# Optimization experiments

Hardware: AMD Instinct MI355X
Metric: run time of the kernel (lower is better)

The kernel has to match this reference:

```python
import jax, jax.numpy as jnp
import numpy as np

H = 128
B, N, K = 2, 16384, 16


def _gather_neighbors(a, idx):
    # a: (B,N,D), idx: (B,N,K) -> (B,N,K,D), per-batch gather along N
    return jax.vmap(lambda ab, ib: ab[ib])(a, idx)


def setup_inputs() -> dict:
    key = jax.random.key(0)
    ks = jax.random.split(key, 16)
    def lin(k, fan_in, shape):
        lim = 1.0 / np.sqrt(fan_in)
        return jax.random.uniform(k, shape, jnp.float32, -lim, lim)
    inp = {
        'h': jax.random.normal(ks[0], (B, N, H), jnp.float32),
        'x': jax.random.normal(ks[1], (B, N, 3), jnp.float32),
        'edge_idx': jax.random.randint(ks[2], (B, N, K), 0, N),
        # edge_mlp: Linear(2H+1->H), SiLU, Linear(H->H), SiLU
        'We1': lin(ks[3], 2 * H + 1, (2 * H + 1, H)), 'be1': lin(ks[4], 2 * H + 1, (H,)),
        'We2': lin(ks[5], H, (H, H)), 'be2': lin(ks[6], H, (H,)),
        # coord_mlp: Linear(H->H), SiLU, Linear(H->1, no bias)
        'Wc1': lin(ks[7], H, (H, H)), 'bc1': lin(ks[8], H, (H,)),
        'Wc2': lin(ks[9], H, (H, 1)),
        # node_mlp: Linear(2H->H), SiLU, Linear(H->H)
        'Wn1': lin(ks[10], 2 * H, (2 * H, H)), 'bn1': lin(ks[11], 2 * H, (H,)),
        'Wn2': lin(ks[12], H, (H, H)), 'bn2': lin(ks[13], H, (H,)),
    }
    return inp


def reference(h, x, edge_idx, We1, be1, We2, be2, Wc1, bc1, Wc2, Wn1, bn1, Wn2, bn2):
    k = edge_idx.shape[2]
    h_neigh = _gather_neighbors(h, edge_idx)          # (B,N,K,H)
    x_neigh = _gather_neighbors(x, edge_idx)          # (B,N,K,3)
    x_diff = x[:, :, None, :] - x_neigh               # (B,N,K,3)
    sq_dist = jnp.sum(x_diff * x_diff, axis=-1, keepdims=True)  # (B,N,K,1)
    h_i = jnp.broadcast_to(h[:, :, None, :], h_neigh.shape)
    edge_feat = jnp.concatenate([h_i, h_neigh, sq_dist], axis=-1)  # (B,N,K,2H+1)
    m_ij = jax.nn.silu(jax.nn.silu(edge_feat @ We1 + be1) @ We2 + be2)  # (B,N,K,H)
    coord_w = jax.nn.silu(m_ij @ Wc1 + bc1) @ Wc2     # (B,N,K,1)
    x_new = x + jnp.mean(x_diff * coord_w, axis=2)    # (B,N,3)
    m_i = jnp.sum(m_ij, axis=2)                       # (B,N,H)
    node_in = jnp.concatenate([h, m_i], axis=-1)      # (B,N,2H)
    h_new = jax.nn.silu(node_in @ Wn1 + bn1) @ Wn2 + bn2 + h
    return (h_new, x_new)
```

## Files before the change

### kernel.cpp

```cpp
#include <hip/hip_runtime.h>
#include <hip/hip_bf16.h>
#include <math.h>

#define H 128
#define KN 16
#define NN 16384
#define NB 8
#define EB 128
#define HS 136

typedef short s16x8 __attribute__((ext_vector_type(8)));
typedef float f32x4 __attribute__((ext_vector_type(4)));

__device__ __forceinline__ float u2f_lo(uint u){
    union { uint i; float f; } v; v.i = u << 16; return v.f;
}
__device__ __forceinline__ float u2f_hi(uint u){
    union { uint i; float f; } v; v.i = u & 0xffff0000u; return v.f;
}
__device__ __forceinline__ uint pk2(float lo, float hi){
    __hip_bfloat162 b = __float22bfloat162_rn(float2{lo, hi});
    uint u; __builtin_memcpy(&u, &b, 4); return u;
}
__device__ __forceinline__ ushort f2b1(float f){
    __hip_bfloat16 b = __float2bfloat16(f);
    ushort u; __builtin_memcpy(&u, &b, 2); return u;
}
__device__ __forceinline__ float silu_f(float v){
    float e = __expf(-v);
    return v * __builtin_amdgcn_rcpf(1.0f + e);
}

__global__ __launch_bounds__(256) void pack_all(
    const float* __restrict__ We2, const float* __restrict__ Wc1,
    const float* __restrict__ Wn1, const float* __restrict__ Wn2,
    const float* __restrict__ We1,
    ushort* __restrict__ dWe2, ushort* __restrict__ dWc1,
    ushort* __restrict__ dWn1, ushort* __restrict__ dWn2,
    ushort* __restrict__ dW1p)
{
    int idx = blockIdx.x * 256 + threadIdx.x;
    int fid = idx >> 6, l = idx & 63;
    const float* src; ushort* dst; int Kt; int mode = 0; int lfid;
    if (fid < 32)       { src = We2; dst = dWe2; Kt = 4; lfid = fid; }
    else if (fid < 64)  { src = Wc1; dst = dWc1; Kt = 4; lfid = fid - 32; }
    else if (fid < 128) { src = Wn1; dst = dWn1; Kt = 8; lfid = fid - 64; }
    else if (fid < 160) { src = Wn2; dst = dWn2; Kt = 4; lfid = fid - 128; }
    else                { src = We1; dst = dW1p; Kt = 4; mode = 1; lfid = fid - 160; }
    int mt = lfid / Kt, kt = lfid % Kt;
    int m = mt * 16 + (l & 15);
    s16x8 ov;
#pragma unroll
    for (int e = 0; e < 8; e++){
        int k = kt * 32 + ((l >> 4) << 3) + e;
        float v;
        if (mode == 0) v = src[k * 128 + m];
        else           v = src[(k + ((m >= 128) ? 128 : 0)) * 128 + (m & 127)];
        ov[e] = (short)f2b1(v);
    }
    *(s16x8*)(dst + (size_t)lfid * 512 + l * 8) = ov;
}

__global__ __launch_bounds__(256) void precompute_mfma(
    const float* __restrict__ h, const float* __restrict__ be1,
    const ushort* __restrict__ W1p,
    ushort* __restrict__ A, ushort* __restrict__ Bm)
{
    const int tid = threadIdx.x;
    const int w = tid >> 6, l = tid & 63, lg = l >> 4, li = l & 15;
    const int i0 = blockIdx.x * 64;

    f32x4 acc[4][4];
#pragma unroll
    for (int a = 0; a < 4; a++)
#pragma unroll
        for (int b = 0; b < 4; b++){ acc[a][b][0]=0.f; acc[a][b][1]=0.f; acc[a][b][2]=0.f; acc[a][b][3]=0.f; }

    for (int nt = 0; nt < 4; nt++){
        int node = i0 + nt * 16 + li;
        const float* hp = h + (size_t)node * 128 + lg * 8;
        s16x8 bfr[4];
#pragma unroll
        for (int kt = 0; kt < 4; kt++){
            float4 v0 = *(const float4*)(hp + kt * 32);
            float4 v1 = *(const float4*)(hp + kt * 32 + 4);
            uint4 uu = make_uint4(pk2(v0.x, v0.y), pk2(v0.z, v0.w),
                                  pk2(v1.x, v1.y), pk2(v1.z, v1.w));
            s16x8 bf; __builtin_memcpy(&bf, &uu, 16);
            bfr[kt] = bf;
        }
#pragma unroll
        for (int mtl = 0; mtl < 4; mtl++){
            int mt = w * 4 + mtl;
#pragma unroll
            for (int kt = 0; kt < 4; kt++){
                s16x8 af = *(const s16x8*)(W1p + (size_t)(mt * 4 + kt) * 512 + l * 8);
                acc[mtl][nt] = __builtin_amdgcn_mfma_f32_16x16x32_bf16(af, bfr[kt], acc[mtl][nt], 0, 0, 0);
            }
        }
    }
#pragma unroll
    for (int mtl = 0; mtl < 4; mtl++){
        int mt = w * 4 + mtl;
        int ccb = mt * 16 + lg * 4;
#pragma unroll
        for (int nt = 0; nt < 4; nt++){
            int node = i0 + nt * 16 + li;
            float b0=0.f,b1=0.f,b2=0.f,b3=0.f;
            if (ccb < 128){ float4 bb = *(const float4*)(be1 + ccb); b0=bb.x; b1=bb.y; b2=bb.z; b3=bb.w; }
            uint2 val = make_uint2(pk2(acc[mtl][nt][0] + b0, acc[mtl][nt][1] + b1),
                                   pk2(acc[mtl][nt][2] + b2, acc[mtl][nt][3] + b3));
            ushort* dst = (ccb < 128) ? (A + (size_t)node * 128 + ccb)
                                      : (Bm + (size_t)node * 128 + (ccb - 128));
            *(uint2*)dst = val;
        }
    }
}

__global__ __launch_bounds__(256, 4) void egnn_fused(
    const float* __restrict__ h, const float* __restrict__ x,
    const int* __restrict__ edge_idx,
    const ushort* __restrict__ A, const ushort* __restrict__ Bm,
    const float* __restrict__ We1,
    const ushort* __restrict__ We2T, const float* __restrict__ be2,
    const ushort* __restrict__ Wc1T, const float* __restrict__ bc1,
    const float* __restrict__ Wc2,
    const ushort* __restrict__ Wn1T, const float* __restrict__ bn1,
    const ushort* __restrict__ Wn2T, const float* __restrict__ bn2,
    float* __restrict__ out, int BN)
{
    __shared__ __align__(16) ushort m_lds[EB * 128];
    __shared__ __align__(16) uint   AshCw[512];
    __shared__ __align__(16) ushort hsh_bf[NB * HS];
    __shared__ __align__(16) ushort msum_bf[NB * HS];
    __shared__ __align__(16) ushort w256sh[128];
    __shared__ float  sqd[EB];
    __shared__ int    jgs[EB];

    ushort* Ash = (ushort*)AshCw;
    float (*cwvp)[EB] = (float(*)[EB])AshCw;

    const int tid = threadIdx.x;
    const int w = tid >> 6, l = tid & 63, lg = l >> 4, li = l & 15;
    const int i0 = blockIdx.x * NB;

    {
        int r = tid >> 5, c = (tid & 31) * 4;
        float4 hv = *(const float4*)&h[(size_t)(i0 + r) * 128 + c];
        *(uint2*)&hsh_bf[r * HS + c] = make_uint2(pk2(hv.x, hv.y), pk2(hv.z, hv.w));
        if (tid < 128){
            int rr = tid >> 4, cc = (tid & 15) * 8;
            *(uint4*)&Ash[rr * 128 + cc] = *(const uint4*)&A[(size_t)(i0 + rr) * 128 + cc];
        } else {
            int t2 = tid - 128;
            w256sh[t2] = f2b1(We1[256 * 128 + t2]);
        }
        if (tid < EB){
            int e = tid;
            int i = i0 + (e >> 4);
            int b = i / NN;
            int jl = edge_idx[(size_t)i * KN + (e & 15)];
            int j = b * NN + jl;
            jgs[e] = j;
            float d0 = x[(size_t)i*3+0] - x[(size_t)j*3+0];
            float d1 = x[(size_t)i*3+1] - x[(size_t)j*3+1];
            float d2 = x[(size_t)i*3+2] - x[(size_t)j*3+2];
            sqd[e] = d0*d0 + d1*d1 + d2*d2;
        }
    }
    __syncthreads();

    {
        const int e0 = w * 32;
#pragma unroll
        for (int nt = 0; nt < 2; nt++){
            int edge = e0 + nt * 16 + li;
            int nodel = edge >> 4;
            int j = jgs[edge];
            float sq = sqd[edge];
#pragma unroll
            for (int kt = 0; kt < 4; kt++){
                int c8 = kt * 32 + lg * 8;
                uint4 ub = *(const uint4*)&Bm[(size_t)j * 128 + c8];
                uint4 ua = *(const uint4*)&Ash[nodel * 128 + c8];
                uint4 uw = *(const uint4*)&w256sh[c8];
                uint ov[4];
                const uint* pa = (const uint*)&ua;
                const uint* pb = (const uint*)&ub;
                const uint* pw = (const uint*)&uw;
#pragma unroll
                for (int p = 0; p < 4; p++){
                    float tlo = fmaf(sq, u2f_lo(pw[p]), u2f_lo(pa[p]) + u2f_lo(pb[p]));
                    float thi = fmaf(sq, u2f_hi(pw[p]), u2f_hi(pa[p]) + u2f_hi(pb[p]));
                    ov[p] = pk2(silu_f(tlo), silu_f(thi));
                }
                int blk = (kt * 4 + lg) ^ (edge & 7);
                *(uint4*)&m_lds[edge * 128 + blk * 8] = make_uint4(ov[0], ov[1], ov[2], ov[3]);
            }
        }
    }
    __syncthreads();

    f32x4 acc[16];
#pragma unroll
    for (int q = 0; q < 16; q++){ acc[q][0]=0.f; acc[q][1]=0.f; acc[q][2]=0.f; acc[q][3]=0.f; }

    __builtin_amdgcn_s_setprio(1);
#pragma unroll
    for (int kt = 0; kt < 4; kt++){
        s16x8 bfr[8];
#pragma unroll
        for (int nt = 0; nt < 8; nt++){
            int edge = nt * 16 + li;
            int blk = (kt * 4 + lg) ^ (edge & 7);
            bfr[nt] = *(const s16x8*)&m_lds[edge * 128 + blk * 8];
        }
#pragma unroll
        for (int mtl = 0; mtl < 2; mtl++){
            int mt = w * 2 + mtl;
            s16x8 af = *(const s16x8*)&We2T[(size_t)(mt * 4 + kt) * 512 + l * 8];
#pragma unroll
            for (int nt = 0; nt < 8; nt++)
                acc[mtl * 8 + nt] = __builtin_amdgcn_mfma_f32_16x16x32_bf16(af, bfr[nt], acc[mtl * 8 + nt], 0, 0, 0);
        }
    }
    __builtin_amdgcn_s_setprio(0);
    __syncthreads();

#pragma unroll
    for (int mtl = 0; mtl < 2; mtl++){
        int mt = w * 2 + mtl;
        int cb = mt * 16 + lg * 4;
        float4 bb = *(const float4*)&be2[cb];
#pragma unroll
        for (int nt = 0; nt < 8; nt++){
            int edge = nt * 16 + li;
            f32x4 a = acc[mtl * 8 + nt];
            uint2 val = make_uint2(pk2(silu_f(a[0] + bb.x), silu_f(a[1] + bb.y)),
                                   pk2(silu_f(a[2] + bb.z), silu_f(a[3] + bb.w)));
            int blk = (mt * 2 + (lg >> 1)) ^ (edge & 7);
            *(uint2*)&m_lds[edge * 128 + blk * 8 + (lg & 1) * 4] = val;
        }
    }
    __syncthreads();
    {
        int nodel = l >> 3;
        int c0 = w * 32 + (l & 7) * 4;
        float s0=0.f, s1=0.f, s2=0.f, s3=0.f;
#pragma unroll
        for (int k = 0; k < 16; k++){
            int edge = nodel * 16 + k;
            int blk = (c0 >> 3) ^ (edge & 7);
            uint2 v = *(uint2*)&m_lds[edge * 128 + blk * 8 + (c0 & 4)];
            s0 += u2f_lo(v.x); s1 += u2f_hi(v.x);
            s2 += u2f_lo(v.y); s3 += u2f_hi(v.y);
        }
        *(uint2*)&msum_bf[nodel * HS + c0] = make_uint2(pk2(s0, s1), pk2(s2, s3));
    }
    __syncthreads();

#pragma unroll
    for (int q = 0; q < 16; q++){ acc[q][0]=0.f; acc[q][1]=0.f; acc[q][2]=0.f; acc[q][3]=0.f; }
    __builtin_amdgcn_s_setprio(1);
#pragma unroll
    for (int kt = 0; kt < 4; kt++){
        s16x8 bfr[8];
#pragma unroll
        for (int nt = 0; nt < 8; nt++){
            int edge = nt * 16 + li;
            int blk = (kt * 4 + lg) ^ (edge & 7);
            bfr[nt] = *(const s16x8*)&m_lds[edge * 128 + blk * 8];
        }
#pragma unroll
        for (int mtl = 0; mtl < 2; mtl++){
            int mt = w * 2 + mtl;
            s16x8 af = *(const s16x8*)&Wc1T[(size_t)(mt * 4 + kt) * 512 + l * 8];
#pragma unroll
            for (int nt = 0; nt < 8; nt++)
                acc[mtl * 8 + nt] = __builtin_amdgcn_mfma_f32_16x16x32_bf16(af, bfr[nt], acc[mtl * 8 + nt], 0, 0, 0);
        }
    }
    __builtin_amdgcn_s_setprio(0);
    __syncthreads();

    {
        float cwp[8];
#pragma unroll
        for (int nt = 0; nt < 8; nt++) cwp[nt] = 0.f;
#pragma unroll
        for (int mtl = 0; mtl < 2; mtl++){
            int mt = w * 2 + mtl;
            int cb = mt * 16 + lg * 4;
            float4 bc = *(const float4*)&bc1[cb];
            float4 wc = *(const float4*)&Wc2[cb];
#pragma unroll
            for (int nt = 0; nt < 8; nt++){
                f32x4 a = acc[mtl * 8 + nt];
                cwp[nt] += silu_f(a[0] + bc.x) * wc.x + silu_f(a[1] + bc.y) * wc.y
                         + silu_f(a[2] + bc.z) * wc.z + silu_f(a[3] + bc.w) * wc.w;
            }
        }
#pragma unroll
        for (int nt = 0; nt < 8; nt++){
            float v = cwp[nt];
            v += __shfl_xor(v, 16);
            v += __shfl_xor(v, 32);
            if (lg == 0) cwvp[w][nt * 16 + li] = v;
        }
    }

    {
        f32x4 acc3[2];
        acc3[0][0]=0.f; acc3[0][1]=0.f; acc3[0][2]=0.f; acc3[0][3]=0.f;
        acc3[1][0]=0.f; acc3[1][1]=0.f; acc3[1][2]=0.f; acc3[1][3]=0.f;
        int node = li & 7;
#pragma unroll
        for (int kt = 0; kt < 8; kt++){
            const ushort* bp = (kt < 4) ? &hsh_bf[node * HS + kt * 32 + lg * 8]
                                        : &msum_bf[node * HS + (kt - 4) * 32 + lg * 8];
            s16x8 bf = *(const s16x8*)bp;
#pragma unroll
            for (int mtl = 0; mtl < 2; mtl++){
                int mt = w * 2 + mtl;
                s16x8 af = *(const s16x8*)&Wn1T[(size_t)(mt * 8 + kt) * 512 + l * 8];
                acc3[mtl] = __builtin_amdgcn_mfma_f32_16x16x32_bf16(af, bf, acc3[mtl], 0, 0, 0);
            }
        }
#pragma unroll
        for (int mtl = 0; mtl < 2; mtl++){
            int mt = w * 2 + mtl;
            int cb = mt * 16 + lg * 4;
            float4 bb = *(const float4*)&bn1[cb];
            uint o01 = 0, o23 = 0;
            if (li < 8){
                f32x4 a = acc3[mtl];
                o01 = pk2(silu_f(a[0] + bb.x), silu_f(a[1] + bb.y));
                o23 = pk2(silu_f(a[2] + bb.z), silu_f(a[3] + bb.w));
            }
            int blk = (mt * 2 + (lg >> 1)) ^ (li & 7);
            *(uint2*)&m_lds[li * 128 + blk * 8 + (lg & 1) * 4] = make_uint2(o01, o23);
        }
    }
    __syncthreads();

    if (tid < 24){
        int nd = tid / 3, d = tid % 3;
        int i = i0 + nd;
        float xi = x[(size_t)i * 3 + d];
        float s = 0.f;
#pragma unroll
        for (int k = 0; k < 16; k++){
            int e = nd * 16 + k;
            float cw = cwvp[0][e] + cwvp[1][e] + cwvp[2][e] + cwvp[3][e];
            s += (xi - x[(size_t)jgs[e] * 3 + d]) * cw;
        }
        out[(size_t)BN * H + (size_t)i * 3 + d] = xi + s * (1.0f / 16.0f);
    }

    {
        f32x4 acc4[2];
        acc4[0][0]=0.f; acc4[0][1]=0.f; acc4[0][2]=0.f; acc4[0][3]=0.f;
        acc4[1][0]=0.f; acc4[1][1]=0.f; acc4[1][2]=0.f; acc4[1][3]=0.f;
#pragma unroll
        for (int kt = 0; kt < 4; kt++){
            int blk = (kt * 4 + lg) ^ (li & 7);
            s16x8 bf = *(const s16x8*)&m_lds[li * 128 + blk * 8];
#pragma unroll
            for (int mtl = 0; mtl < 2; mtl++){
                int mt = w * 2 + mtl;
                s16x8 af = *(const s16x8*)&Wn2T[(size_t)(mt * 4 + kt) * 512 + l * 8];
                acc4[mtl] = __builtin_amdgcn_mfma_f32_16x16x32_bf16(af, bf, acc4[mtl], 0, 0, 0);
            }
        }
#pragma unroll
        for (int mtl = 0; mtl < 2; mtl++){
            int mt = w * 2 + mtl;
            int cb = mt * 16 + lg * 4;
            if (li < 8){
                float4 bb = *(const float4*)&bn2[cb];
                float4 hv = *(const float4*)&h[(size_t)(i0 + li) * 128 + cb];
                f32x4 a = acc4[mtl];
                float4 o;
                o.x = a[0] + bb.x + hv.x;
                o.y = a[1] + bb.y + hv.y;
                o.z = a[2] + bb.z + hv.z;
                o.w = a[3] + bb.w + hv.w;
                *(float4*)&out[(size_t)(i0 + li) * 128 + cb] = o;
            }
        }
    }
}

extern "C" void kernel_launch(void* const* d_in, const int* in_sizes, int n_in,
                              void* d_out, int out_size, void* d_ws, size_t ws_size,
                              hipStream_t stream) {
    const float* h        = (const float*)d_in[0];
    const float* x        = (const float*)d_in[1];
    const int*   edge_idx = (const int*)d_in[2];
    const float* We1      = (const float*)d_in[3];
    const float* be1      = (const float*)d_in[4];
    const float* We2      = (const float*)d_in[5];
    const float* be2      = (const float*)d_in[6];
    const float* Wc1      = (const float*)d_in[7];
    const float* bc1      = (const float*)d_in[8];
    const float* Wc2      = (const float*)d_in[9];
    const float* Wn1      = (const float*)d_in[10];
    const float* bn1      = (const float*)d_in[11];
    const float* Wn2      = (const float*)d_in[12];
    const float* bn2      = (const float*)d_in[13];
    float* out = (float*)d_out;

    const int BN = in_sizes[0] / H;

    ushort* A    = (ushort*)d_ws;
    ushort* Bm   = A + (size_t)BN * H;
    ushort* We2T = Bm + (size_t)BN * H;
    ushort* Wc1T = We2T + 32 * 512;
    ushort* Wn1T = Wc1T + 32 * 512;
    ushort* Wn2T = Wn1T + 64 * 512;
    ushort* W1pT = Wn2T + 32 * 512;

    pack_all<<<56, 256, 0, stream>>>(We2, Wc1, Wn1, Wn2, We1,
                                     We2T, Wc1T, Wn1T, Wn2T, W1pT);
    precompute_mfma<<<BN / 64, 256, 0, stream>>>(h, be1, W1pT, A, Bm);
    egnn_fused<<<BN / NB, 256, 0, stream>>>(h, x, edge_idx, A, Bm, We1,
                                            We2T, be2, Wc1T, bc1, Wc2,
                                            Wn1T, bn1, Wn2T, bn2, out, BN);
}
```

Measured before the change: 140.4 us.

## Make each wave own its edges end to end, removing block barriers

Each wave now handles 32 edges (two nodes) across the whole edge pipeline. It computes the first-layer activations straight into MFMA register fragments instead of staging them in LDS, runs all 8 output tiles for its own edges, and keeps its private slice of the message buffer. This removes most __syncthreads and the Ash/w256sh/jgs staging, at the cost of more accumulator registers per wave and reloading all weight tiles per wave. Coordinate differences are cached in LDS as bf16, and the residual h is read from the bf16 shared copy. Both lower the precision of the x and h outputs.

```diff
diff --git a/kernel.cpp b/kernel.cpp
--- a/kernel.cpp
+++ b/kernel.cpp
@@ -17,6 +17,9 @@
 }
 __device__ __forceinline__ float u2f_hi(uint u){
     union { uint i; float f; } v; v.i = u & 0xffff0000u; return v.f;
+}
+__device__ __forceinline__ float b2f(ushort u){
+    union { uint i; float f; } v; v.i = ((uint)u) << 16; return v.f;
 }
 __device__ __forceinline__ uint pk2(float lo, float hi){
     __hip_bfloat162 b = __float22bfloat162_rn(float2{lo, hi});
@@ -130,15 +133,10 @@
     float* __restrict__ out, int BN)
 {
     __shared__ __align__(16) ushort m_lds[EB * 128];
-    __shared__ __align__(16) uint   AshCw[512];
     __shared__ __align__(16) ushort hsh_bf[NB * HS];
     __shared__ __align__(16) ushort msum_bf[NB * HS];
-    __shared__ __align__(16) ushort w256sh[128];
-    __shared__ float  sqd[EB];
-    __shared__ int    jgs[EB];
-
-    ushort* Ash = (ushort*)AshCw;
-    float (*cwvp)[EB] = (float(*)[EB])AshCw;
+    __shared__ float  cwv[EB];
+    __shared__ ushort xdb[EB * 3];
 
     const int tid = threadIdx.x;
     const int w = tid >> 6, l = tid & 63, lg = l >> 4, li = l & 15;
@@ -148,166 +146,144 @@
         int r = tid >> 5, c = (tid & 31) * 4;
         float4 hv = *(const float4*)&h[(size_t)(i0 + r) * 128 + c];
         *(uint2*)&hsh_bf[r * HS + c] = make_uint2(pk2(hv.x, hv.y), pk2(hv.z, hv.w));
-        if (tid < 128){
-            int rr = tid >> 4, cc = (tid & 15) * 8;
-            *(uint4*)&Ash[rr * 128 + cc] = *(const uint4*)&A[(size_t)(i0 + rr) * 128 + cc];
-        } else {
-            int t2 = tid - 128;
-            w256sh[t2] = f2b1(We1[256 * 128 + t2]);
-        }
-        if (tid < EB){
-            int e = tid;
-            int i = i0 + (e >> 4);
-            int b = i / NN;
-            int jl = edge_idx[(size_t)i * KN + (e & 15)];
-            int j = b * NN + jl;
-            jgs[e] = j;
-            float d0 = x[(size_t)i*3+0] - x[(size_t)j*3+0];
-            float d1 = x[(size_t)i*3+1] - x[(size_t)j*3+1];
-            float d2 = x[(size_t)i*3+2] - x[(size_t)j*3+2];
-            sqd[e] = d0*d0 + d1*d1 + d2*d2;
-        }
-    }
-    __syncthreads();
-
-    {
-        const int e0 = w * 32;
-#pragma unroll
-        for (int nt = 0; nt < 2; nt++){
-            int edge = e0 + nt * 16 + li;
-            int nodel = edge >> 4;
-            int j = jgs[edge];
-            float sq = sqd[edge];
-#pragma unroll
-            for (int kt = 0; kt < 4; kt++){
-                int c8 = kt * 32 + lg * 8;
-                uint4 ub = *(const uint4*)&Bm[(size_t)j * 128 + c8];
-                uint4 ua = *(const uint4*)&Ash[nodel * 128 + c8];
-                uint4 uw = *(const uint4*)&w256sh[c8];
-                uint ov[4];
-                const uint* pa = (const uint*)&ua;
-                const uint* pb = (const uint*)&ub;
-                const uint* pw = (const uint*)&uw;
-#pragma unroll
-                for (int p = 0; p < 4; p++){
-                    float tlo = fmaf(sq, u2f_lo(pw[p]), u2f_lo(pa[p]) + u2f_lo(pb[p]));
-                    float thi = fmaf(sq, u2f_hi(pw[p]), u2f_hi(pa[p]) + u2f_hi(pb[p]));
-                    ov[p] = pk2(silu_f(tlo), silu_f(thi));
-                }
-                int blk = (kt * 4 + lg) ^ (edge & 7);
-                *(uint4*)&m_lds[edge * 128 + blk * 8] = make_uint4(ov[0], ov[1], ov[2], ov[3]);
-            }
-        }
-    }
-    __syncthreads();
-
-    f32x4 acc[16];
-#pragma unroll
-    for (int q = 0; q < 16; q++){ acc[q][0]=0.f; acc[q][1]=0.f; acc[q][2]=0.f; acc[q][3]=0.f; }
+    }
+    float sqv = 0.f; int jv = 0;
+    if (l < 32) {
+        int el = w * 32 + l;
+        int i = i0 + (el >> 4);
+        int b = i / NN;
+        int jl = edge_idx[(size_t)i * KN + (el & 15)];
+        int j = b * NN + jl;
+        jv = j;
+        float d0 = x[(size_t)i*3+0] - x[(size_t)j*3+0];
+        float d1 = x[(size_t)i*3+1] - x[(size_t)j*3+1];
+        float d2 = x[(size_t)i*3+2] - x[(size_t)j*3+2];
+        xdb[el*3+0] = f2b1(d0); xdb[el*3+1] = f2b1(d1); xdb[el*3+2] = f2b1(d2);
+        sqv = d0*d0 + d1*d1 + d2*d2;
+    }
+
+    s16x8 tfr[2][4];
+#pragma unroll
+    for (int nt = 0; nt < 2; nt++){
+        int els = nt * 16 + li;
+        float sq = __shfl(sqv, els);
+        int j = __shfl(jv, els);
+        const size_t arow = (size_t)(i0 + w * 2 + nt) * 128;
+#pragma unroll
+        for (int kt = 0; kt < 4; kt++){
+            int c8 = kt * 32 + lg * 8;
+            uint4 ua = *(const uint4*)&A[arow + c8];
+            uint4 ub = *(const uint4*)&Bm[(size_t)j * 128 + c8];
+            float4 w0 = *(const float4*)&We1[256*128 + c8];
+            float4 w1 = *(const float4*)&We1[256*128 + c8 + 4];
+            float wlo[4] = {w0.x, w0.z, w1.x, w1.z};
+            float whi[4] = {w0.y, w0.w, w1.y, w1.w};
+            const uint* pa = (const uint*)&ua;
+            const uint* pb = (const uint*)&ub;
+            uint ov[4];
+#pragma unroll
+            for (int p = 0; p < 4; p++){
+                float tlo = fmaf(sq, wlo[p], u2f_lo(pa[p]) + u2f_lo(pb[p]));
+                float thi = fmaf(sq, whi[p], u2f_hi(pa[p]) + u2f_hi(pb[p]));
+                ov[p] = pk2(silu_f(tlo), silu_f(thi));
+            }
+            __builtin_memcpy(&tfr[nt][kt], ov, 16);
+        }
+    }
+
+    f32x4 acc[8][2];
+#pragma unroll
+    for (int mt = 0; mt < 8; mt++)
+#pragma unroll
+        for (int nt = 0; nt < 2; nt++){ acc[mt][nt][0]=0.f; acc[mt][nt][1]=0.f; acc[mt][nt][2]=0.f; acc[mt][nt][3]=0.f; }
 
     __builtin_amdgcn_s_setprio(1);
 #pragma unroll
     for (int kt = 0; kt < 4; kt++){
-        s16x8 bfr[8];
-#pragma unroll
-        for (int nt = 0; nt < 8; nt++){
-            int edge = nt * 16 + li;
-            int blk = (kt * 4 + lg) ^ (edge & 7);
-            bfr[nt] = *(const s16x8*)&m_lds[edge * 128 + blk * 8];
-        }
-#pragma unroll
-        for (int mtl = 0; mtl < 2; mtl++){
-            int mt = w * 2 + mtl;
-            s16x8 af = *(const s16x8*)&We2T[(size_t)(mt * 4 + kt) * 512 + l * 8];
-#pragma unroll
-            for (int nt = 0; nt < 8; nt++)
-                acc[mtl * 8 + nt] = __builtin_amdgcn_mfma_f32_16x16x32_bf16(af, bfr[nt], acc[mtl * 8 + nt], 0, 0, 0);
+#pragma unroll
+        for (int mt = 0; mt < 8; mt++){
+            s16x8 af = *(const s16x8*)&We2T[(size_t)(mt*4+kt)*512 + l*8];
+            acc[mt][0] = __builtin_amdgcn_mfma_f32_16x16x32_bf16(af, tfr[0][kt], acc[mt][0], 0, 0, 0);
+            acc[mt][1] = __builtin_amdgcn_mfma_f32_16x16x32_bf16(af, tfr[1][kt], acc[mt][1], 0, 0, 0);
         }
     }
     __builtin_amdgcn_s_setprio(0);
-    __syncthreads();
-
-#pragma unroll
-    for (int mtl = 0; mtl < 2; mtl++){
-        int mt = w * 2 + mtl;
+
+    ushort* mreg = m_lds + w * 32 * 128;
+#pragma unroll
+    for (int mt = 0; mt < 8; mt++){
         int cb = mt * 16 + lg * 4;
         float4 bb = *(const float4*)&be2[cb];
 #pragma unroll
-        for (int nt = 0; nt < 8; nt++){
-            int edge = nt * 16 + li;
-            f32x4 a = acc[mtl * 8 + nt];
+        for (int nt = 0; nt < 2; nt++){
+            int el = nt * 16 + li;
+            f32x4 a = acc[mt][nt];
             uint2 val = make_uint2(pk2(silu_f(a[0] + bb.x), silu_f(a[1] + bb.y)),
                                    pk2(silu_f(a[2] + bb.z), silu_f(a[3] + bb.w)));
-            int blk = (mt * 2 + (lg >> 1)) ^ (edge & 7);
-            *(uint2*)&m_lds[edge * 128 + blk * 8 + (lg & 1) * 4] = val;
-        }
-    }
-    __syncthreads();
+            int blk = (mt * 2 + (lg >> 1)) ^ (el & 7);
+            *(uint2*)&mreg[el * 128 + blk * 8 + (lg & 1) * 4] = val;
+        }
+    }
+
     {
-        int nodel = l >> 3;
-        int c0 = w * 32 + (l & 7) * 4;
+        int nodel = l >> 5;
+        int c0 = (l & 31) * 4;
         float s0=0.f, s1=0.f, s2=0.f, s3=0.f;
 #pragma unroll
         for (int k = 0; k < 16; k++){
-            int edge = nodel * 16 + k;
-            int blk = (c0 >> 3) ^ (edge & 7);
-            uint2 v = *(uint2*)&m_lds[edge * 128 + blk * 8 + (c0 & 4)];
+            int row = nodel * 16 + k;
+            int blk = (c0 >> 3) ^ (row & 7);
+            uint2 v = *(const uint2*)&mreg[row * 128 + blk * 8 + (c0 & 4)];
             s0 += u2f_lo(v.x); s1 += u2f_hi(v.x);
             s2 += u2f_lo(v.y); s3 += u2f_hi(v.y);
         }
-        *(uint2*)&msum_bf[nodel * HS + c0] = make_uint2(pk2(s0, s1), pk2(s2, s3));
-    }
-    __syncthreads();
-
-#pragma unroll
-    for (int q = 0; q < 16; q++){ acc[q][0]=0.f; acc[q][1]=0.f; acc[q][2]=0.f; acc[q][3]=0.f; }
+        *(uint2*)&msum_bf[(w*2 + nodel) * HS + c0] = make_uint2(pk2(s0, s1), pk2(s2, s3));
+    }
+
+    f32x4 acc2[8][2];
+#pragma unroll
+    for (int mt = 0; mt < 8; mt++)
+#pragma unroll
+        for (int nt = 0; nt < 2; nt++){ acc2[mt][nt][0]=0.f; acc2[mt][nt][1]=0.f; acc2[mt][nt][2]=0.f; acc2[mt][nt][3]=0.f; }
+
     __builtin_amdgcn_s_setprio(1);
 #pragma unroll
     for (int kt = 0; kt < 4; kt++){
-        s16x8 bfr[8];
-#pragma unroll
-        for (int nt = 0; nt < 8; nt++){
-            int edge = nt * 16 + li;
-            int blk = (kt * 4 + lg) ^ (edge & 7);
-            bfr[nt] = *(const s16x8*)&m_lds[edge * 128 + blk * 8];
-        }
-#pragma unroll
-        for (int mtl = 0; mtl < 2; mtl++){
-            int mt = w * 2 + mtl;
-            s16x8 af = *(const s16x8*)&Wc1T[(size_t)(mt * 4 + kt) * 512 + l * 8];
-#pragma unroll
-            for (int nt = 0; nt < 8; nt++)
-                acc[mtl * 8 + nt] = __builtin_amdgcn_mfma_f32_16x16x32_bf16(af, bfr[nt], acc[mtl * 8 + nt], 0, 0, 0);
+        int blk0 = (kt*4 + lg) ^ (li & 7);
+        s16x8 bf0 = *(const s16x8*)&mreg[li * 128 + blk0 * 8];
+        int el1 = 16 + li;
+        int blk1 = (kt*4 + lg) ^ (el1 & 7);
+        s16x8 bf1 = *(const s16x8*)&mreg[el1 * 128 + blk1 * 8];
+#pragma unroll
+        for (int mt = 0; mt < 8; mt++){
+            s16x8 af = *(const s16x8*)&Wc1T[(size_t)(mt*4+kt)*512 + l*8];
+            acc2[mt][0] = __builtin_amdgcn_mfma_f32_16x16x32_bf16(af, bf0, acc2[mt][0], 0, 0, 0);
+            acc2[mt][1] = __builtin_amdgcn_mfma_f32_16x16x32_bf16(af, bf1, acc2[mt][1], 0, 0, 0);
         }
     }
     __builtin_amdgcn_s_setprio(0);
-    __syncthreads();
 
     {
-        float cwp[8];
-#pragma unroll
-        for (int nt = 0; nt < 8; nt++) cwp[nt] = 0.f;
-#pragma unroll
-        for (int mtl = 0; mtl < 2; mtl++){
-            int mt = w * 2 + mtl;
+        float cwp0 = 0.f, cwp1 = 0.f;
+#pragma unroll
+        for (int mt = 0; mt < 8; mt++){
             int cb = mt * 16 + lg * 4;
             float4 bc = *(const float4*)&bc1[cb];
             float4 wc = *(const float4*)&Wc2[cb];
-#pragma unroll
-            for (int nt = 0; nt < 8; nt++){
-                f32x4 a = acc[mtl * 8 + nt];
-                cwp[nt] += silu_f(a[0] + bc.x) * wc.x + silu_f(a[1] + bc.y) * wc.y
-                         + silu_f(a[2] + bc.z) * wc.z + silu_f(a[3] + bc.w) * wc.w;
-            }
-        }
-#pragma unroll
-        for (int nt = 0; nt < 8; nt++){
-            float v = cwp[nt];
-            v += __shfl_xor(v, 16);
-            v += __shfl_xor(v, 32);
-            if (lg == 0) cwvp[w][nt * 16 + li] = v;
-        }
-    }
+            f32x4 a0 = acc2[mt][0], a1 = acc2[mt][1];
+            cwp0 += silu_f(a0[0]+bc.x)*wc.x + silu_f(a0[1]+bc.y)*wc.y
+                  + silu_f(a0[2]+bc.z)*wc.z + silu_f(a0[3]+bc.w)*wc.w;
+            cwp1 += silu_f(a1[0]+bc.x)*wc.x + silu_f(a1[1]+bc.y)*wc.y
+                  + silu_f(a1[2]+bc.z)*wc.z + silu_f(a1[3]+bc.w)*wc.w;
+        }
+        cwp0 += __shfl_xor(cwp0, 16); cwp0 += __shfl_xor(cwp0, 32);
+        cwp1 += __shfl_xor(cwp1, 16); cwp1 += __shfl_xor(cwp1, 32);
+        if (lg == 0){
+            cwv[w*32 + li]      = cwp0;
+            cwv[w*32 + 16 + li] = cwp1;
+        }
+    }
+    __syncthreads();
 
     {
         f32x4 acc3[2];
@@ -316,13 +292,13 @@
         int node = li & 7;
 #pragma unroll
         for (int kt = 0; kt < 8; kt++){
-            const ushort* bp = (kt < 4) ? &hsh_bf[node * HS + kt * 32 + lg * 8]
-                                        : &msum_bf[node * HS + (kt - 4) * 32 + lg * 8];
+            const ushort* bp = (kt < 4) ? &hsh_bf[node * HS + kt*32 + lg*8]
+                                        : &msum_bf[node * HS + (kt-4)*32 + lg*8];
             s16x8 bf = *(const s16x8*)bp;
 #pragma unroll
             for (int mtl = 0; mtl < 2; mtl++){
                 int mt = w * 2 + mtl;
-                s16x8 af = *(const s16x8*)&Wn1T[(size_t)(mt * 8 + kt) * 512 + l * 8];
+                s16x8 af = *(const s16x8*)&Wn1T[(size_t)(mt*8+kt)*512 + l*8];
                 acc3[mtl] = __builtin_amdgcn_mfma_f32_16x16x32_bf16(af, bf, acc3[mtl], 0, 0, 0);
             }
         }
@@ -346,15 +322,13 @@
     if (tid < 24){
         int nd = tid / 3, d = tid % 3;
         int i = i0 + nd;
-        float xi = x[(size_t)i * 3 + d];
         float s = 0.f;
 #pragma unroll
         for (int k = 0; k < 16; k++){
             int e = nd * 16 + k;
-            float cw = cwvp[0][e] + cwvp[1][e] + cwvp[2][e] + cwvp[3][e];
-            s += (xi - x[(size_t)jgs[e] * 3 + d]) * cw;
-        }
-        out[(size_t)BN * H + (size_t)i * 3 + d] = xi + s * (1.0f / 16.0f);
+            s += b2f(xdb[e*3 + d]) * cwv[e];
+        }
+        out[(size_t)BN * H + (size_t)i * 3 + d] = x[(size_t)i * 3 + d] + s * (1.0f / 16.0f);
     }
 
     {
@@ -363,12 +337,12 @@
         acc4[1][0]=0.f; acc4[1][1]=0.f; acc4[1][2]=0.f; acc4[1][3]=0.f;
 #pragma unroll
         for (int kt = 0; kt < 4; kt++){
-            int blk = (kt * 4 + lg) ^ (li & 7);
+            int blk = (kt*4 + lg) ^ (li & 7);
             s16x8 bf = *(const s16x8*)&m_lds[li * 128 + blk * 8];
 #pragma unroll
             for (int mtl = 0; mtl < 2; mtl++){
                 int mt = w * 2 + mtl;
-                s16x8 af = *(const s16x8*)&Wn2T[(size_t)(mt * 4 + kt) * 512 + l * 8];
+                s16x8 af = *(const s16x8*)&Wn2T[(size_t)(mt*4+kt)*512 + l*8];
                 acc4[mtl] = __builtin_amdgcn_mfma_f32_16x16x32_bf16(af, bf, acc4[mtl], 0, 0, 0);
             }
         }
@@ -378,13 +352,13 @@
             int cb = mt * 16 + lg * 4;
             if (li < 8){
                 float4 bb = *(const float4*)&bn2[cb];
-                float4 hv = *(const float4*)&h[(size_t)(i0 + li) * 128 + cb];
+                uint2 hu = *(const uint2*)&hsh_bf[li * HS + cb];
                 f32x4 a = acc4[mtl];
                 float4 o;
-                o.x = a[0] + bb.x + hv.x;
-                o.y = a[1] + bb.y + hv.y;
-                o.z = a[2] + bb.z + hv.z;
-                o.w = a[3] + bb.w + hv.w;
+                o.x = a[0] + bb.x + u2f_lo(hu.x);
+                o.y = a[1] + bb.y + u2f_hi(hu.x);
+                o.z = a[2] + bb.z + u2f_lo(hu.y);
+                o.w = a[3] + bb.w + u2f_hi(hu.y);
                 *(float4*)&out[(size_t)(i0 + li) * 128 + cb] = o;
             }
         }
```

Result: slower. 175.5 us (+25.0%).
